# Kernel tuning notes

Measured on AMD Instinct MI355X. Metric: run time of the kernel, lower is better.

The kernel has to match this reference:

```python
import jax, jax.numpy as jnp
import numpy as np

HIDDEN_DIM = 512
SCALE = HIDDEN_DIM ** (-0.5)


def setup_inputs() -> dict:
    key = jax.random.key(0)
    kx, kw = jax.random.split(key)
    x = jax.random.normal(kx, (4, 4096, HIDDEN_DIM), dtype=jnp.float32)
    # nn.Linear weight is [out, in]; y = x @ W.T. We store W in torch layout.
    Wq = jax.random.normal(kw, (HIDDEN_DIM, HIDDEN_DIM), dtype=jnp.float32) * (HIDDEN_DIM ** -0.5)
    return {"x": x, "Wq": Wq}


def reference(x, Wq):
    # Faithful to source: q, k, v all use the SAME q_matrix projection.
    q = jnp.einsum("bcd,ed->bce", x, Wq)  # [B, C, D]
    k = q
    v = q
    scores = jnp.einsum("bcd,bed->bce", q, k) * SCALE  # [B, C, C]
    attn = jax.nn.softmax(scores, axis=-1)
    # dropout p=0.0 -> identity
    y = jnp.einsum("bce,bed->bcd", attn, v)  # [B, C, D]
    return y
```

## Files before the change

kernel.cpp:

```cpp
#include <hip/hip_runtime.h>
#include <stdint.h>

typedef unsigned int u32;
typedef unsigned short u16;
typedef __attribute__((ext_vector_type(8))) short bf16x8;
typedef __attribute__((ext_vector_type(4))) float f32x4;

#define B_ 4
#define S_ 4096
#define D_ 512
#define SCALE_ 0.04419417382415922f

__device__ __forceinline__ u16 f2b(float f) {
  u32 u = __builtin_bit_cast(u32, f);
  return (u16)((u + 0x7FFFu + ((u >> 16) & 1u)) >> 16);
}
__device__ __forceinline__ u16 f2b_fast(float f) {
  u32 u = __builtin_bit_cast(u32, f);
  return (u16)((u + 0x8000u) >> 16);
}
__device__ __forceinline__ void gld16(const void* g, void* l) {
  __builtin_amdgcn_global_load_lds(
      (const __attribute__((address_space(1))) u32*)g,
      (__attribute__((address_space(3))) u32*)l, 16, 0, 0);
}

__global__ __launch_bounds__(256, 1) void qprep(
    const float* __restrict__ W, u16* __restrict__ Wb) {
  int i = (blockIdx.x * 256 + threadIdx.x) * 4;
  float4 a = *(const float4*)(W + i);
  ushort4 o;
  o.x = f2b(a.x); o.y = f2b(a.y); o.z = f2b(a.z); o.w = f2b(a.w);
  *(ushort4*)(Wb + i) = o;
}

__global__ __launch_bounds__(256, 1) void qproj(
    const float* __restrict__ X, const u16* __restrict__ Wb,
    u16* __restrict__ Qr, u16* __restrict__ Qt) {
  __shared__ __align__(16) u16 Wt[2][512 * 64];
  const int tid = threadIdx.x;
  const int wave = tid >> 6, lane = tid & 63;
  const int m16 = lane & 15, quad = lane >> 4;
  const int r0 = blockIdx.x * 64;

  const float* xrow = X + (size_t)(r0 + wave * 16 + m16) * D_;
  bf16x8 af[16];
#pragma unroll
  for (int ks = 0; ks < 16; ++ks) {
    const float* ap = xrow + ks * 32 + quad * 8;
    float4 a0 = ((const float4*)ap)[0];
    float4 a1 = ((const float4*)ap)[1];
    bf16x8 v;
    v[0] = (short)f2b(a0.x); v[1] = (short)f2b(a0.y);
    v[2] = (short)f2b(a0.z); v[3] = (short)f2b(a0.w);
    v[4] = (short)f2b(a1.x); v[5] = (short)f2b(a1.y);
    v[6] = (short)f2b(a1.z); v[7] = (short)f2b(a1.w);
    af[ks] = v;
  }

  f32x4 acc[32];
#pragma unroll
  for (int i = 0; i < 32; ++i) acc[i] = f32x4{};

  auto stage = [&](int kc, int buf) {
#pragma unroll
    for (int t = 0; t < 16; ++t) {
      int e0 = (wave * 16 + t) * 8;
      int e = e0 + (lane >> 3);
      int gb = ((lane & 7) - e) & 7;
      gld16(Wb + (size_t)e * D_ + kc * 64 + gb * 8, &Wt[buf][e0 * 64]);
    }
  };

  stage(0, 0);
  __syncthreads();

  for (int kc = 0; kc < 8; ++kc) {
    if (kc < 7) stage(kc + 1, (kc + 1) & 1);
    const u16* wb = &Wt[kc & 1][0];
#pragma unroll
    for (int kk = 0; kk < 2; ++kk) {
      int jb = quad + 4 * kk;
      bf16x8 a = af[kc * 2 + kk];
#pragma unroll
      for (int nt = 0; nt < 32; ++nt) {
        int e = m16 + nt * 16;
        bf16x8 bf = *(const bf16x8*)(wb + e * 64 + ((jb + e) & 7) * 8);
        acc[nt] = __builtin_amdgcn_mfma_f32_16x16x32_bf16(a, bf, acc[nt], 0, 0, 0);
      }
    }
    __syncthreads();
  }

  const int b = r0 >> 12;
  const int s0 = (r0 & (S_ - 1)) + wave * 16 + quad * 4;
  const int grow = r0 + wave * 16 + quad * 4;
#pragma unroll
  for (int nt = 0; nt < 32; ++nt) {
    int e = nt * 16 + m16;
    u16 h0 = f2b(acc[nt][0]), h1 = f2b(acc[nt][1]);
    u16 h2 = f2b(acc[nt][2]), h3 = f2b(acc[nt][3]);
    Qr[(size_t)(grow + 0) * D_ + e] = h0;
    Qr[(size_t)(grow + 1) * D_ + e] = h1;
    Qr[(size_t)(grow + 2) * D_ + e] = h2;
    Qr[(size_t)(grow + 3) * D_ + e] = h3;
    uint2 pv;
    pv.x = (u32)h0 | ((u32)h1 << 16);
    pv.y = (u32)h2 | ((u32)h3 << 16);
    *(uint2*)(&Qt[((size_t)(b * D_ + e)) * S_ + s0]) = pv;
  }
}

__global__ __launch_bounds__(256, 1) void flashattn(
    const u16* __restrict__ Qrow, const u16* __restrict__ Qt,
    float* __restrict__ Out) {
  __shared__ __align__(16) u16 Kt[64 * 512];
  __shared__ __align__(16) u16 Vt[512 * 64];
  __shared__ __align__(16) u16 Pl[4][16 * 88];

  const int tid = threadIdx.x;
  const int wave = tid >> 6, lane = tid & 63;
  const int m16 = lane & 15, quad = lane >> 4;
  const int qt = blockIdx.x, bb = blockIdx.y;
  const u16* Qb  = Qrow + (size_t)bb * S_ * D_;
  const u16* Qtb = Qt   + (size_t)bb * D_ * S_;

  auto stageK = [&](int kt) {
    const u16* src = Qb + (size_t)(kt * 64) * D_;
#pragma unroll
    for (int t = 0; t < 16; ++t) {
      int n = wave * 16 + t;
      int gb = (lane & ~7) | ((lane + n) & 7);
      gld16(src + (size_t)n * D_ + gb * 8, &Kt[n * 512]);
    }
  };
  auto stageV = [&](int kt) {
    const u16* vsrc = Qtb + kt * 64;
#pragma unroll
    for (int t = 0; t < 16; ++t) {
      int d0 = (wave * 16 + t) * 8;
      int d  = d0 + (lane >> 3);
      int gb = ((lane & 7) + d) & 7;
      gld16(vsrc + (size_t)d * S_ + gb * 8, &Vt[d0 * 64]);
    }
  };

  bf16x8 qf[16];
  {
    const u16* qp = Qb + (size_t)(qt * 64 + wave * 16 + m16) * D_ + quad * 8;
#pragma unroll
    for (int ks = 0; ks < 16; ++ks) qf[ks] = *(const bf16x8*)(qp + ks * 32);
  }

  bf16x8 onesf;
#pragma unroll
  for (int j = 0; j < 8; ++j) onesf[j] = (short)0x3F80;

  f32x4 o[32];
#pragma unroll
  for (int i = 0; i < 32; ++i) o[i] = f32x4{};
  f32x4 ol = f32x4{};
  float mrow[4] = {-1e30f, -1e30f, -1e30f, -1e30f};
  u16* pw = &Pl[wave][0];

  stageK(0);
  __syncthreads();

  for (int kt = 0; kt < 64; ++kt) {
    stageV(kt);

    f32x4 sv[4];
#pragma unroll
    for (int nt = 0; nt < 4; ++nt) {
      f32x4 a = f32x4{};
      int n = m16 + nt * 16;
      const u16* kr = &Kt[n * 512];
#pragma unroll
      for (int ks = 0; ks < 16; ++ks) {
        int jb = quad + 4 * ks;
        int ib = (jb & ~7) | ((jb - n) & 7);
        bf16x8 bf = *(const bf16x8*)(kr + ib * 8);
        a = __builtin_amdgcn_mfma_f32_16x16x32_bf16(qf[ks], bf, a, 0, 0, 0);
      }
      sv[nt] = a;
    }

    float mnew[4], alpha[4];
    int grew = 0;
#pragma unroll
    for (int r = 0; r < 4; ++r) {
      float t = fmaxf(fmaxf(sv[0][r], sv[1][r]), fmaxf(sv[2][r], sv[3][r]));
      t = fmaxf(t, __shfl_xor(t, 1));
      t = fmaxf(t, __shfl_xor(t, 2));
      t = fmaxf(t, __shfl_xor(t, 4));
      t = fmaxf(t, __shfl_xor(t, 8));
      float mn = fmaxf(mrow[r], t);
      mnew[r] = mn;
      grew |= (mn > mrow[r]);
      alpha[r] = __expf((mrow[r] - mn) * SCALE_);
      mrow[r] = mn;
    }
#pragma unroll
    for (int nt = 0; nt < 4; ++nt) {
#pragma unroll
      for (int r = 0; r < 4; ++r) {
        float p = __expf((sv[nt][r] - mnew[r]) * SCALE_);
        pw[(quad * 4 + r) * 88 + nt * 16 + m16] = f2b_fast(p);
      }
    }

    __syncthreads();

    if (kt < 63) stageK(kt + 1);

    if (__ballot(grew) != 0ull) {
#pragma unroll
      for (int dt = 0; dt < 32; ++dt) {
        o[dt][0] *= alpha[0]; o[dt][1] *= alpha[1];
        o[dt][2] *= alpha[2]; o[dt][3] *= alpha[3];
      }
      ol[0] *= alpha[0]; ol[1] *= alpha[1];
      ol[2] *= alpha[2]; ol[3] *= alpha[3];
    }

#pragma unroll
    for (int ks2 = 0; ks2 < 2; ++ks2) {
      bf16x8 pf = *(const bf16x8*)(pw + m16 * 88 + ks2 * 32 + quad * 8);
      int ib = ((quad + 4 * ks2) - m16) & 7;
#pragma unroll
      for (int dt = 0; dt < 32; ++dt) {
        int d = m16 + dt * 16;
        bf16x8 vf = *(const bf16x8*)(&Vt[d * 64 + ib * 8]);
        o[dt] = __builtin_amdgcn_mfma_f32_16x16x32_bf16(pf, vf, o[dt], 0, 0, 0);
      }
      ol = __builtin_amdgcn_mfma_f32_16x16x32_bf16(pf, onesf, ol, 0, 0, 0);
    }

    __syncthreads();
  }

  float inv[4];
#pragma unroll
  for (int r = 0; r < 4; ++r) inv[r] = 1.f / ol[r];
  const int row0 = qt * 64 + wave * 16 + quad * 4;
#pragma unroll
  for (int dt = 0; dt < 32; ++dt) {
    int col = dt * 16 + m16;
    size_t base = ((size_t)bb * S_ + row0) * D_ + col;
    Out[base]           = o[dt][0] * inv[0];
    Out[base + D_]      = o[dt][1] * inv[1];
    Out[base + 2 * D_]  = o[dt][2] * inv[2];
    Out[base + 3 * D_]  = o[dt][3] * inv[3];
  }
}

extern "C" void kernel_launch(void* const* d_in, const int* in_sizes, int n_in,
                              void* d_out, int out_size, void* d_ws, size_t ws_size,
                              hipStream_t stream) {
  (void)in_sizes; (void)n_in; (void)out_size; (void)ws_size;
  const float* X = (const float*)d_in[0];
  const float* W = (const float*)d_in[1];
  float* Out = (float*)d_out;
  u16* Qr = (u16*)d_ws;
  u16* Qt = Qr + (size_t)B_ * S_ * D_;
  u16* Wb = Qt + (size_t)B_ * D_ * S_;

  qprep<<<dim3(256), dim3(256), 0, stream>>>(W, Wb);
  qproj<<<dim3(256), dim3(256), 0, stream>>>(X, Wb, Qr, Qt);
  flashattn<<<dim3(64, 4), dim3(256), 0, stream>>>(Qr, Qt, Out);
}
```

Measured before the change: 356.5 us.

## Split KV loop across two wave groups per block with merged softmax state

The flash-attention block grows to 512 threads as two 4-wave groups. Each group handles alternate 32-key tiles of the sequence using its own K/V shared buffers, and the groups merge their partial outputs, row maxima and sums through shared memory at the end. The grid is flattened so that consecutive blocks map to interleaved batches and query tiles. The aim is more waves per CU to hide latency, at the cost of smaller MFMA work per sync, extra LDS traffic for the final merge, and higher register pressure under launch_bounds(512,2).

```diff
diff --git a/kernel.cpp b/kernel.cpp
--- a/kernel.cpp
+++ b/kernel.cpp
@@ -111,43 +111,52 @@
   }
 }
 
-__global__ __launch_bounds__(256, 1) void flashattn(
+__global__ __launch_bounds__(512, 2) void flashattn(
     const u16* __restrict__ Qrow, const u16* __restrict__ Qt,
     float* __restrict__ Out) {
-  __shared__ __align__(16) u16 Kt[64 * 512];
-  __shared__ __align__(16) u16 Vt[512 * 64];
-  __shared__ __align__(16) u16 Pl[4][16 * 88];
+  __shared__ __align__(16) u16 KV[2][32768];
+  __shared__ __align__(16) u16 Pl[8][640];
 
   const int tid = threadIdx.x;
   const int wave = tid >> 6, lane = tid & 63;
+  const int g = wave >> 2, wv = wave & 3;
   const int m16 = lane & 15, quad = lane >> 4;
-  const int qt = blockIdx.x, bb = blockIdx.y;
+
+  const int f = blockIdx.x;
+  const int x8 = f & 7;
+  const int bb = x8 >> 1;
+  const int qt = ((f >> 3) << 1) | (x8 & 1);
+
   const u16* Qb  = Qrow + (size_t)bb * S_ * D_;
   const u16* Qtb = Qt   + (size_t)bb * D_ * S_;
+  u16* Kt = &KV[g][0];
+  u16* Vt = &KV[g][16384];
 
   auto stageK = [&](int kt) {
-    const u16* src = Qb + (size_t)(kt * 64) * D_;
-#pragma unroll
-    for (int t = 0; t < 16; ++t) {
-      int n = wave * 16 + t;
+    const u16* src = Qb + (size_t)(kt * 32) * D_;
+#pragma unroll
+    for (int t = 0; t < 8; ++t) {
+      int n = wv * 8 + t;
       int gb = (lane & ~7) | ((lane + n) & 7);
       gld16(src + (size_t)n * D_ + gb * 8, &Kt[n * 512]);
     }
   };
   auto stageV = [&](int kt) {
-    const u16* vsrc = Qtb + kt * 64;
-#pragma unroll
-    for (int t = 0; t < 16; ++t) {
-      int d0 = (wave * 16 + t) * 8;
-      int d  = d0 + (lane >> 3);
-      int gb = ((lane & 7) + d) & 7;
-      gld16(vsrc + (size_t)d * S_ + gb * 8, &Vt[d0 * 64]);
+    const u16* vsrc = Qtb + kt * 32;
+#pragma unroll
+    for (int t = 0; t < 8; ++t) {
+      int d0 = (wv * 8 + t) * 16;
+      int d  = d0 + (lane >> 2);
+      int kb = ((lane & 3) - d) & 3;
+      gld16(vsrc + (size_t)d * S_ + kb * 8, &Vt[d0 * 32]);
     }
   };
+
+  stageK(g);
 
   bf16x8 qf[16];
   {
-    const u16* qp = Qb + (size_t)(qt * 64 + wave * 16 + m16) * D_ + quad * 8;
+    const u16* qp = Qb + (size_t)(qt * 64 + wv * 16 + m16) * D_ + quad * 8;
 #pragma unroll
     for (int ks = 0; ks < 16; ++ks) qf[ks] = *(const bf16x8*)(qp + ks * 32);
   }
@@ -163,15 +172,16 @@
   float mrow[4] = {-1e30f, -1e30f, -1e30f, -1e30f};
   u16* pw = &Pl[wave][0];
 
-  stageK(0);
   __syncthreads();
 
-  for (int kt = 0; kt < 64; ++kt) {
+  for (int i = 0; i < 64; ++i) {
+    const int kt = 2 * i + g;
+
     stageV(kt);
 
-    f32x4 sv[4];
-#pragma unroll
-    for (int nt = 0; nt < 4; ++nt) {
+    f32x4 sv[2];
+#pragma unroll
+    for (int nt = 0; nt < 2; ++nt) {
       f32x4 a = f32x4{};
       int n = m16 + nt * 16;
       const u16* kr = &Kt[n * 512];
@@ -189,7 +199,7 @@
     int grew = 0;
 #pragma unroll
     for (int r = 0; r < 4; ++r) {
-      float t = fmaxf(fmaxf(sv[0][r], sv[1][r]), fmaxf(sv[2][r], sv[3][r]));
+      float t = fmaxf(sv[0][r], sv[1][r]);
       t = fmaxf(t, __shfl_xor(t, 1));
       t = fmaxf(t, __shfl_xor(t, 2));
       t = fmaxf(t, __shfl_xor(t, 4));
@@ -201,17 +211,16 @@
       mrow[r] = mn;
     }
 #pragma unroll
-    for (int nt = 0; nt < 4; ++nt) {
+    for (int nt = 0; nt < 2; ++nt)
 #pragma unroll
       for (int r = 0; r < 4; ++r) {
         float p = __expf((sv[nt][r] - mnew[r]) * SCALE_);
-        pw[(quad * 4 + r) * 88 + nt * 16 + m16] = f2b_fast(p);
-      }
-    }
+        pw[(quad * 4 + r) * 40 + nt * 16 + m16] = f2b_fast(p);
+      }
 
     __syncthreads();
 
-    if (kt < 63) stageK(kt + 1);
+    if (i < 63) stageK(kt + 2);
 
     if (__ballot(grew) != 0ull) {
 #pragma unroll
@@ -223,34 +232,53 @@
       ol[2] *= alpha[2]; ol[3] *= alpha[3];
     }
 
-#pragma unroll
-    for (int ks2 = 0; ks2 < 2; ++ks2) {
-      bf16x8 pf = *(const bf16x8*)(pw + m16 * 88 + ks2 * 32 + quad * 8);
-      int ib = ((quad + 4 * ks2) - m16) & 7;
-#pragma unroll
-      for (int dt = 0; dt < 32; ++dt) {
-        int d = m16 + dt * 16;
-        bf16x8 vf = *(const bf16x8*)(&Vt[d * 64 + ib * 8]);
-        o[dt] = __builtin_amdgcn_mfma_f32_16x16x32_bf16(pf, vf, o[dt], 0, 0, 0);
-      }
-      ol = __builtin_amdgcn_mfma_f32_16x16x32_bf16(pf, onesf, ol, 0, 0, 0);
-    }
+    bf16x8 pf = *(const bf16x8*)(pw + m16 * 40 + quad * 8);
+#pragma unroll
+    for (int dt = 0; dt < 32; ++dt) {
+      int d = m16 + dt * 16;
+      int s = (quad + d) & 3;
+      bf16x8 vf = *(const bf16x8*)(&Vt[d * 32 + s * 8]);
+      o[dt] = __builtin_amdgcn_mfma_f32_16x16x32_bf16(pf, vf, o[dt], 0, 0, 0);
+    }
+    ol = __builtin_amdgcn_mfma_f32_16x16x32_bf16(pf, onesf, ol, 0, 0, 0);
 
     __syncthreads();
   }
 
-  float inv[4];
-#pragma unroll
-  for (int r = 0; r < 4; ++r) inv[r] = 1.f / ol[r];
-  const int row0 = qt * 64 + wave * 16 + quad * 4;
-#pragma unroll
-  for (int dt = 0; dt < 32; ++dt) {
-    int col = dt * 16 + m16;
-    size_t base = ((size_t)bb * S_ + row0) * D_ + col;
-    Out[base]           = o[dt][0] * inv[0];
-    Out[base + D_]      = o[dt][1] * inv[1];
-    Out[base + 2 * D_]  = o[dt][2] * inv[2];
-    Out[base + 3 * D_]  = o[dt][3] * inv[3];
+  if (g == 1) {
+    f32x4* ob = (f32x4*)&KV[0][0];
+    float* ml = (float*)&Pl[0][0] + (wv * 64 + lane) * 8;
+    int base = wv * 2048 + lane;
+#pragma unroll
+    for (int dt = 0; dt < 32; ++dt) ob[base + dt * 64] = o[dt];
+#pragma unroll
+    for (int r = 0; r < 4; ++r) { ml[r] = mrow[r]; ml[4 + r] = ol[r]; }
+  }
+  __syncthreads();
+  if (g == 0) {
+    const f32x4* ob = (const f32x4*)&KV[0][0];
+    const float* ml = (const float*)&Pl[0][0] + (wv * 64 + lane) * 8;
+    float aA[4], aB[4], inv[4];
+#pragma unroll
+    for (int r = 0; r < 4; ++r) {
+      float mB = ml[r], lB = ml[4 + r];
+      float m = fmaxf(mrow[r], mB);
+      aA[r] = __expf((mrow[r] - m) * SCALE_);
+      aB[r] = __expf((mB - m) * SCALE_);
+      inv[r] = 1.f / (ol[r] * aA[r] + lB * aB[r]);
+    }
+    const int row0 = qt * 64 + wv * 16 + quad * 4;
+    int base = wv * 2048 + lane;
+#pragma unroll
+    for (int dt = 0; dt < 32; ++dt) {
+      f32x4 oB = ob[base + dt * 64];
+      int col = dt * 16 + m16;
+      size_t obase = ((size_t)bb * S_ + row0) * D_ + col;
+      Out[obase]          = (o[dt][0] * aA[0] + oB[0] * aB[0]) * inv[0];
+      Out[obase + D_]     = (o[dt][1] * aA[1] + oB[1] * aB[1]) * inv[1];
+      Out[obase + 2 * D_] = (o[dt][2] * aA[2] + oB[2] * aB[2]) * inv[2];
+      Out[obase + 3 * D_] = (o[dt][3] * aA[3] + oB[3] * aB[3]) * inv[3];
+    }
   }
 }
 
@@ -267,5 +295,5 @@
 
   qprep<<<dim3(256), dim3(256), 0, stream>>>(W, Wb);
   qproj<<<dim3(256), dim3(256), 0, stream>>>(X, Wb, Qr, Qt);
-  flashattn<<<dim3(64, 4), dim3(256), 0, stream>>>(Qr, Qt, Out);
-}
+  flashattn<<<dim3(256), dim3(512), 0, stream>>>(Qr, Qt, Out);
+}
```

After: 543.5 us. 1.52x slower.

## Double-buffer K/V tiles with 32-key blocks and vmcnt-based barriers in flash attention

Applied to the files above, without the earlier changes.

Halves the key tile from 64 to 32 rows so K and V can each be double-buffered in LDS, and prefetches the next V and the K two steps ahead while computing on the current buffer. The __syncthreads calls are replaced by explicit s_waitcnt vmcnt plus s_barrier, so only the loads that are actually needed are waited on. This is meant to hide global-to-LDS load latency behind MFMA work. In exchange there are twice as many iterations, each with more softmax/rescale overhead per key, and correctness depends on the hand-counted vmcnt values.

```diff
diff --git a/kernel.cpp b/kernel.cpp
--- a/kernel.cpp
+++ b/kernel.cpp
@@ -24,6 +24,12 @@
       (const __attribute__((address_space(1))) u32*)g,
       (__attribute__((address_space(3))) u32*)l, 16, 0, 0);
 }
+
+#define WAITBAR(N)                                                     \
+  do {                                                                 \
+    asm volatile("s_waitcnt vmcnt(" #N ")\n\ts_barrier" ::: "memory"); \
+    __builtin_amdgcn_sched_barrier(0);                                 \
+  } while (0)
 
 __global__ __launch_bounds__(256, 1) void qprep(
     const float* __restrict__ W, u16* __restrict__ Wb) {
@@ -114,9 +120,9 @@
 __global__ __launch_bounds__(256, 1) void flashattn(
     const u16* __restrict__ Qrow, const u16* __restrict__ Qt,
     float* __restrict__ Out) {
-  __shared__ __align__(16) u16 Kt[64 * 512];
-  __shared__ __align__(16) u16 Vt[512 * 64];
-  __shared__ __align__(16) u16 Pl[4][16 * 88];
+  __shared__ __align__(16) u16 Kt[2][32 * 512];
+  __shared__ __align__(16) u16 Vt[2][512 * 32];
+  __shared__ __align__(16) u16 Pl[4][16 * 40];
 
   const int tid = threadIdx.x;
   const int wave = tid >> 6, lane = tid & 63;
@@ -125,23 +131,23 @@
   const u16* Qb  = Qrow + (size_t)bb * S_ * D_;
   const u16* Qtb = Qt   + (size_t)bb * D_ * S_;
 
-  auto stageK = [&](int kt) {
-    const u16* src = Qb + (size_t)(kt * 64) * D_;
-#pragma unroll
-    for (int t = 0; t < 16; ++t) {
-      int n = wave * 16 + t;
+  auto stageK = [&](int kt, int buf) {
+    const u16* src = Qb + (size_t)(kt * 32) * D_;
+#pragma unroll
+    for (int t = 0; t < 8; ++t) {
+      int n = wave * 8 + t;
       int gb = (lane & ~7) | ((lane + n) & 7);
-      gld16(src + (size_t)n * D_ + gb * 8, &Kt[n * 512]);
+      gld16(src + (size_t)n * D_ + gb * 8, &Kt[buf][n * 512]);
     }
   };
-  auto stageV = [&](int kt) {
-    const u16* vsrc = Qtb + kt * 64;
-#pragma unroll
-    for (int t = 0; t < 16; ++t) {
-      int d0 = (wave * 16 + t) * 8;
-      int d  = d0 + (lane >> 3);
-      int gb = ((lane & 7) + d) & 7;
-      gld16(vsrc + (size_t)d * S_ + gb * 8, &Vt[d0 * 64]);
+  auto stageV = [&](int kt, int buf) {
+    const u16* vsrc = Qtb + kt * 32;
+#pragma unroll
+    for (int t = 0; t < 8; ++t) {
+      int d0 = (wave * 8 + t) * 16;
+      int d  = d0 + (lane >> 2);
+      int kb = ((lane & 3) - d) & 3;
+      gld16(vsrc + (size_t)d * S_ + kb * 8, &Vt[buf][d0 * 32]);
     }
   };
 
@@ -163,18 +169,22 @@
   float mrow[4] = {-1e30f, -1e30f, -1e30f, -1e30f};
   u16* pw = &Pl[wave][0];
 
-  stageK(0);
-  __syncthreads();
-
-  for (int kt = 0; kt < 64; ++kt) {
-    stageV(kt);
-
-    f32x4 sv[4];
-#pragma unroll
-    for (int nt = 0; nt < 4; ++nt) {
+  stageK(0, 0);
+  stageV(0, 0);
+  stageK(1, 1);
+
+  for (int kt = 0; kt < 128; ++kt) {
+    const int buf = kt & 1;
+
+    if (kt < 127) { WAITBAR(16); } else { WAITBAR(8); }
+    if (kt < 127) stageV(kt + 1, buf ^ 1);
+
+    f32x4 sv[2];
+#pragma unroll
+    for (int nt = 0; nt < 2; ++nt) {
       f32x4 a = f32x4{};
       int n = m16 + nt * 16;
-      const u16* kr = &Kt[n * 512];
+      const u16* kr = &Kt[buf][n * 512];
 #pragma unroll
       for (int ks = 0; ks < 16; ++ks) {
         int jb = quad + 4 * ks;
@@ -189,7 +199,7 @@
     int grew = 0;
 #pragma unroll
     for (int r = 0; r < 4; ++r) {
-      float t = fmaxf(fmaxf(sv[0][r], sv[1][r]), fmaxf(sv[2][r], sv[3][r]));
+      float t = fmaxf(sv[0][r], sv[1][r]);
       t = fmaxf(t, __shfl_xor(t, 1));
       t = fmaxf(t, __shfl_xor(t, 2));
       t = fmaxf(t, __shfl_xor(t, 4));
@@ -201,17 +211,16 @@
       mrow[r] = mn;
     }
 #pragma unroll
-    for (int nt = 0; nt < 4; ++nt) {
+    for (int nt = 0; nt < 2; ++nt) {
 #pragma unroll
       for (int r = 0; r < 4; ++r) {
         float p = __expf((sv[nt][r] - mnew[r]) * SCALE_);
-        pw[(quad * 4 + r) * 88 + nt * 16 + m16] = f2b_fast(p);
-      }
-    }
-
-    __syncthreads();
-
-    if (kt < 63) stageK(kt + 1);
+        pw[(quad * 4 + r) * 40 + nt * 16 + m16] = f2b_fast(p);
+      }
+    }
+
+    if (kt < 127) { WAITBAR(16); } else { WAITBAR(0); }
+    if (kt < 126) stageK(kt + 2, buf);
 
     if (__ballot(grew) != 0ull) {
 #pragma unroll
@@ -223,20 +232,15 @@
       ol[2] *= alpha[2]; ol[3] *= alpha[3];
     }
 
-#pragma unroll
-    for (int ks2 = 0; ks2 < 2; ++ks2) {
-      bf16x8 pf = *(const bf16x8*)(pw + m16 * 88 + ks2 * 32 + quad * 8);
-      int ib = ((quad + 4 * ks2) - m16) & 7;
-#pragma unroll
-      for (int dt = 0; dt < 32; ++dt) {
-        int d = m16 + dt * 16;
-        bf16x8 vf = *(const bf16x8*)(&Vt[d * 64 + ib * 8]);
-        o[dt] = __builtin_amdgcn_mfma_f32_16x16x32_bf16(pf, vf, o[dt], 0, 0, 0);
-      }
-      ol = __builtin_amdgcn_mfma_f32_16x16x32_bf16(pf, onesf, ol, 0, 0, 0);
-    }
-
-    __syncthreads();
+    bf16x8 pf = *(const bf16x8*)(pw + m16 * 40 + quad * 8);
+#pragma unroll
+    for (int dt = 0; dt < 32; ++dt) {
+      int d = m16 + dt * 16;
+      int s = (quad + d) & 3;
+      bf16x8 vf = *(const bf16x8*)(&Vt[buf][d * 32 + s * 8]);
+      o[dt] = __builtin_amdgcn_mfma_f32_16x16x32_bf16(pf, vf, o[dt], 0, 0, 0);
+    }
+    ol = __builtin_amdgcn_mfma_f32_16x16x32_bf16(pf, onesf, ol, 0, 0, 0);
   }
 
   float inv[4];
```

Result: slower. 505.0 us (+41.7%).
